# Performance work log

Hardware: AMD Instinct MI355X
Metric: run time of the kernel (lower is better)

## Reference

```python
import jax, jax.numpy as jnp
import numpy as np

B, L, DIM = 2, 1024, 1024
H, DH = 16, 64          # n_heads, dim_per_head
GS = 1                  # group_size
T = 3 * GS              # triplet heads (last T heads, head_choice==0)
HN = H - T              # normal heads
DG = DH * GS            # triplet 'pseudo-head' dim
SCALE = 1.0 / np.sqrt(DH)


def setup_inputs() -> dict:
    key = jax.random.key(0)
    ks = jax.random.split(key, 12)
    s = 0.02
    return {
        'query': jax.random.normal(ks[0], (B, L, DIM), jnp.float32),
        'key':   jax.random.normal(ks[1], (B, L, DIM), jnp.float32),
        'value': jax.random.normal(ks[2], (B, L, DIM), jnp.float32),
        'mask':  jnp.ones((B, L), dtype=jnp.int32),
        'Wq': jax.random.normal(ks[3], (DIM, DIM), jnp.float32) * s,
        'bq': jnp.zeros((DIM,), jnp.float32),
        'Wk': jax.random.normal(ks[4], (DIM, DIM), jnp.float32) * s,
        'bk': jnp.zeros((DIM,), jnp.float32),
        'Wv': jax.random.normal(ks[5], (DIM, DIM), jnp.float32) * s,
        'bv': jnp.zeros((DIM,), jnp.float32),
        'Wo': jax.random.normal(ks[6], (DIM, DIM), jnp.float32) * s,
        'bo': jnp.zeros((DIM,), jnp.float32),
    }


def _split_heads(x, W, b):
    # x: [B,L,DIM] -> [B,H,L,DH]
    return (x @ W.T + b).reshape(B, L, H, DH).transpose(0, 2, 1, 3)


def _triplet_reshape(x):
    # [B,T,L,DH] -> [B,L,T,DH] -> [B,L,DG,3] -> [B,DG,L,3]
    return x.transpose(0, 2, 1, 3).reshape(B, L, DG, 3).transpose(0, 2, 1, 3)


def reference(query, key, value, mask, Wq, bq, Wk, bk, Wv, bv, Wo, bo):
    q = _split_heads(query, Wq, bq)
    k = _split_heads(key, Wk, bk)
    v = _split_heads(value, Wv, bv)

    # head split: last T heads go to the triplet branch (head_choice == 0)
    qn, qt = q[:, :HN], q[:, HN:]
    kn, kt = k[:, :HN], k[:, HN:]
    vn, vt = v[:, :HN], v[:, HN:]

    # ---- triplet branch (layer in Tlayers) ----
    qtr = _triplet_reshape(qt)   # [B,DG,L,3]
    ktr = _triplet_reshape(kt)
    vtr = _triplet_reshape(vt)

    # key2_flag==1: key_triplet2 = clone; permute_type=[2] => roll index by 1 along L
    idx = jnp.roll(jnp.arange(L), 1)
    kt2 = ktr[:, :, idx, :]
    K_cross = jnp.cross(ktr, kt2, axis=-1)                 # [B,DG,L,3]

    attn_t = jnp.einsum('bdlt,bdmt->bdlm', qtr, K_cross)   # [B,DG,L,L]
    # permute_back==0, random_flag==0: inverse permutation along last dim
    inv = jnp.argsort(idx)
    attn_t = attn_t[..., inv]
    # absolute_flag==1
    attn_t = jnp.abs(attn_t)

    # ---- normal attention ----
    scores = jnp.einsum('bhld,bhmd->bhlm', qn * SCALE, kn)  # [B,HN,L,L]
    pad = (mask == 0)[:, None, None, :]
    scores = jnp.where(pad, -jnp.inf, scores)
    w = jax.nn.softmax(scores, axis=-1)                     # dropout p=0

    wt = jax.nn.softmax(attn_t * SCALE, axis=-1)            # [B,DG,L,L]

    ctx = jnp.einsum('bhlm,bhmd->bhld', w, vn)              # [B,HN,L,DH]
    ctx = ctx.transpose(0, 2, 1, 3).reshape(B, L, HN * DH)

    ctx_t = jnp.einsum('bdlm,bdmt->bdlt', wt, vtr)          # [B,DG,L,3]
    ctx_t = ctx_t.transpose(0, 2, 1, 3).reshape(B, L, DG * 3)

    context = jnp.concatenate([ctx, ctx_t], axis=-1)        # [B,L,DIM]
    return context @ Wo.T + bo
```

## Files before the change

kernel.cpp:

```cpp
#include <hip/hip_runtime.h>

#define L_SEQ 1024
typedef unsigned short ush;
typedef __attribute__((ext_vector_type(8))) short short8;
typedef __attribute__((ext_vector_type(4))) float f32x4;

#define MFMA __builtin_amdgcn_mfma_f32_16x16x32_bf16

#define Q_PRESCALE 0.18033688011112042f

__device__ __forceinline__ ush f2bf(float x) {
  union { float f; unsigned u; } c; c.f = x;
  unsigned r = c.u + 0x7FFF + ((c.u >> 16) & 1);
  return (ush)(r >> 16);
}
__device__ __forceinline__ float bf2f(ush h) {
  union { unsigned u; float f; } c; c.u = ((unsigned)h) << 16;
  return c.f;
}
__device__ __forceinline__ void gload16(const void* g, void* l) {
  __builtin_amdgcn_global_load_lds(
      (const __attribute__((address_space(1))) unsigned*)g,
      (__attribute__((address_space(3))) unsigned*)l, 16, 0, 0);
}

struct SplitA {
  const float* s0; const float* s1; const float* s2; const float* s3;
  const float* s4; const float* s5; const float* s6;
  ush* d0; ush* d1; ush* d2; ush* d3; ush* d4; ush* d5; ush* d6;
};
__global__ __launch_bounds__(256) void split_all(SplitA a) {
  const int ti = blockIdx.y;
  const float* s; ush* d; int n;
  switch (ti) {
    case 0: s = a.s0; d = a.d0; n = 1 << 21; break;
    case 1: s = a.s1; d = a.d1; n = 1 << 21; break;
    case 2: s = a.s2; d = a.d2; n = 1 << 21; break;
    case 3: s = a.s3; d = a.d3; n = 1 << 20; break;
    case 4: s = a.s4; d = a.d4; n = 1 << 20; break;
    case 5: s = a.s5; d = a.d5; n = 1 << 20; break;
    default: s = a.s6; d = a.d6; n = 1 << 20; break;
  }
  int i = (blockIdx.x * 256 + threadIdx.x) * 8;
  if (i >= n) return;
  float4 x0 = *(const float4*)(s + i);
  float4 x1 = *(const float4*)(s + i + 4);
  float xs[8] = {x0.x, x0.y, x0.z, x0.w, x1.x, x1.y, x1.z, x1.w};
  ush h[8], l[8];
  #pragma unroll
  for (int j = 0; j < 8; j++) {
    h[j] = f2bf(xs[j]);
    l[j] = f2bf(xs[j] - bf2f(h[j]));
  }
  ushort4 h0 = {h[0], h[1], h[2], h[3]}, h1 = {h[4], h[5], h[6], h[7]};
  ushort4 l0 = {l[0], l[1], l[2], l[3]}, l1 = {l[4], l[5], l[6], l[7]};
  *(ushort4*)(d + i) = h0;     *(ushort4*)(d + i + 4) = h1;
  *(ushort4*)(d + n + i) = l0; *(ushort4*)(d + n + i + 4) = l1;
}

template <int DBUF>
__global__ __launch_bounds__(256) void gemm_sp(
    const ush* __restrict__ Abase, long AzStride, long Aplane,
    const ush* __restrict__ Bbase, long BzStride,
    const float* __restrict__ b0, const float* __restrict__ b1,
    const float* __restrict__ b2,
    float* __restrict__ Yf, ush* __restrict__ Pbase) {
  __shared__ __align__(16) ush lds[DBUF ? 49152 : 24576];
  const int t = threadIdx.x;
  const int z = blockIdx.z;
  const ush* A = Abase + (size_t)z * AzStride;
  const ush* B = Bbase + (size_t)z * BzStride;
  const float* bias = (z == 0) ? b0 : (z == 1) ? b1 : b2;
  const long Bplane = 1024 * 1024;
  const int r0 = blockIdx.x * 128;
  const int n0 = blockIdx.y * 64;
  const int wid = t >> 6, lane = t & 63;
  const int wr = wid >> 1, wc = wid & 1;
  const int sr = t >> 3, ss = t & 7;
  const int sd = ss ^ (sr & 7);
  const int fr = lane & 15, fk = lane >> 4;

  f32x4 acc[4][2];
  #pragma unroll
  for (int mf = 0; mf < 4; mf++)
    #pragma unroll
    for (int nf = 0; nf < 2; nf++)
      acc[mf][nf] = (f32x4){0.f, 0.f, 0.f, 0.f};

  const ush* Ag = A + (size_t)(r0 + sr) * 1024 + sd * 8;
  const ush* Bg = B + (size_t)(n0 + sr) * 1024 + sd * 8;

  auto stage = [&](ush* Lb, int k0) {
    #pragma unroll
    for (int p = 0; p < 2; p++)
      #pragma unroll
      for (int c = 0; c < 4; c++)
        gload16(Ag + (size_t)p * Aplane + (size_t)c * 32 * 1024 + k0,
                Lb + p * 8192 + (c * 256 + t) * 8);
    #pragma unroll
    for (int p = 0; p < 2; p++)
      #pragma unroll
      for (int c = 0; c < 2; c++)
        gload16(Bg + (size_t)p * Bplane + (size_t)c * 32 * 1024 + k0,
                Lb + 16384 + p * 4096 + (c * 256 + t) * 8);
  };
  auto compute = [&](const ush* Lb) {
    #pragma unroll
    for (int g = 0; g < 2; g++) {
      short8 ah[4], al[4], bh[2], bl[2];
      const int sl = ((g * 4 + fk) ^ (fr & 7)) * 8;
      #pragma unroll
      for (int mf = 0; mf < 4; mf++) {
        int row = wr * 64 + mf * 16 + fr;
        ah[mf] = *(const short8*)(Lb + row * 64 + sl);
        al[mf] = *(const short8*)(Lb + 8192 + row * 64 + sl);
      }
      #pragma unroll
      for (int nf = 0; nf < 2; nf++) {
        int row = wc * 32 + nf * 16 + fr;
        bh[nf] = *(const short8*)(Lb + 16384 + row * 64 + sl);
        bl[nf] = *(const short8*)(Lb + 20480 + row * 64 + sl);
      }
      #pragma unroll
      for (int mf = 0; mf < 4; mf++)
        #pragma unroll
        for (int nf = 0; nf < 2; nf++) {
          acc[mf][nf] = MFMA(ah[mf], bh[nf], acc[mf][nf], 0, 0, 0);
          acc[mf][nf] = MFMA(ah[mf], bl[nf], acc[mf][nf], 0, 0, 0);
          acc[mf][nf] = MFMA(al[mf], bh[nf], acc[mf][nf], 0, 0, 0);
        }
    }
  };

  if constexpr (DBUF) {
    stage(lds, 0);
    __syncthreads();
    for (int k0 = 0; k0 < 1024; k0 += 64) {
      const int cur = (k0 >> 6) & 1;
      if (k0 + 64 < 1024) stage(lds + (cur ^ 1) * 24576, k0 + 64);
      compute(lds + cur * 24576);
      __syncthreads();
    }
  } else {
    for (int k0 = 0; k0 < 1024; k0 += 64) {
      __syncthreads();
      stage(lds, k0);
      __syncthreads();
      compute(lds);
    }
  }

  const float oscale = (z == 0) ? Q_PRESCALE : 1.0f;
  ush* Ph = Pbase ? (Pbase + (size_t)z * 4194304) : (ush*)0;
  ush* Pl = Ph ? Ph + 2097152 : (ush*)0;
  #pragma unroll
  for (int nf = 0; nf < 2; nf++) {
    const int col = n0 + wc * 32 + nf * 16 + fr;
    const float bb = bias[col];
    #pragma unroll
    for (int mf = 0; mf < 4; mf++) {
      const int rowb = r0 + wr * 64 + mf * 16 + fk * 4;
      if (Yf) {
        #pragma unroll
        for (int r = 0; r < 4; r++)
          Yf[(size_t)(rowb + r) * 1024 + col] = acc[mf][nf][r] + bb;
      } else if (z != 2) {
        #pragma unroll
        for (int r = 0; r < 4; r++) {
          float v = (acc[mf][nf][r] + bb) * oscale;
          ush hv = f2bf(v);
          Ph[(size_t)(rowb + r) * 1024 + col] = hv;
          Pl[(size_t)(rowb + r) * 1024 + col] = f2bf(v - bf2f(hv));
        }
      } else {
        ushort4 hv;
        #pragma unroll
        for (int r = 0; r < 4; r++)
          ((ush*)&hv)[r] = f2bf(acc[mf][nf][r] + bb);
        *(ushort4*)&Ph[(size_t)col * 2048 + rowb] = hv;
      }
    }
  }
}

__global__ __launch_bounds__(256) void trip_kc(
    const ush* __restrict__ kh, const ush* __restrict__ kl,
    ush* __restrict__ kc4g) {
  const int t = threadIdx.x;
  const int m = blockIdx.x * 256 + t;
  const int d = blockIdx.y, b = blockIdx.z;
  const int col = 832 + 3 * d;
  size_t r0 = (size_t)(b * 1024 + m) * 1024 + col;
  size_t r1 = (size_t)(b * 1024 + ((m + 1) & 1023)) * 1024 + col;
  float c0 = bf2f(kh[r0]) + bf2f(kl[r0]);
  float c1 = bf2f(kh[r0 + 1]) + bf2f(kl[r0 + 1]);
  float c2 = bf2f(kh[r0 + 2]) + bf2f(kl[r0 + 2]);
  float a0 = bf2f(kh[r1]) + bf2f(kl[r1]);
  float a1 = bf2f(kh[r1 + 1]) + bf2f(kl[r1 + 1]);
  float a2 = bf2f(kh[r1 + 2]) + bf2f(kl[r1 + 2]);
  ushort4 o;
  o.x = f2bf(a1 * c2 - a2 * c1);
  o.y = f2bf(a2 * c0 - a0 * c2);
  o.z = f2bf(a0 * c1 - a1 * c0);
  o.w = 0;
  *(ushort4*)(kc4g + ((size_t)(b * 64 + d) * 1024 + m) * 4) = o;
}

struct NormLds {
  ush Kh[2][4096];
  ush Kl[2][4096];
  ush Vt[2][4096];
  unsigned Pb[4][16][20];
};
struct TripLds {
  ush KC[4096];
  ush VT[4 * 1040];
  ush PB[4][16][36];
};
union FusedLds { NormLds n; TripLds t; };

__global__ __launch_bounds__(256) void attn_fused(
    const ush* __restrict__ qh, const ush* __restrict__ ql,
    const ush* __restrict__ kh, const ush* __restrict__ kl,
    const ush* __restrict__ vth, const ush* __restrict__ kc4g,
    ush* __restrict__ ctxh, ush* __restrict__ ctxl) {
  __shared__ __align__(16) FusedLds L;
  const int t = threadIdx.x;
  const int bid = blockIdx.x;
  const int lane = t & 63, w = t >> 6;
  const int c = lane & 15, g = lane >> 4;

  if (bid < 416) {
    const int l0 = (bid & 15) * 64;
    const int rem = bid >> 4;
    const int h = rem % 13, b = rem / 13;
    const int hoff = h * 64;
    const int srow = t >> 3, sg = t & 7;

    short8 ah[2], al[2];
    {
      size_t qbase = (size_t)(b * 1024 + l0 + w * 16 + c) * 1024 + hoff + g * 8;
      ah[0] = *(const short8*)(qh + qbase);
      ah[1] = *(const short8*)(qh + qbase + 32);
      al[0] = *(const short8*)(ql + qbase);
      al[1] = *(const short8*)(ql + qbase + 32);
    }
    auto stageKV = [&](int buf, int m0) {
      #pragma unroll
      for (int cc = 0; cc < 2; cc++) {
        int row = cc * 32 + srow;
        int slot = sg ^ (row & 7);
        size_t srck = (size_t)(b * 1024 + m0 + row) * 1024 + hoff + slot * 8;
        gload16(kh + srck, &L.n.Kh[buf][row * 64 + sg * 8]);
        gload16(kl + srck, &L.n.Kl[buf][row * 64 + sg * 8]);
        size_t srcv = (size_t)(hoff + row) * 2048 + b * 1024 + m0 + slot * 8;
        gload16(vth + srcv, &L.n.Vt[buf][row * 64 + sg * 8]);
      }
    };
    stageKV(0, 0);
    __syncthreads();

    const short8 ones = {0x3F80, 0x3F80, 0x3F80, 0x3F80,
                         0x3F80, 0x3F80, 0x3F80, 0x3F80};
    f32x4 acc[4];
    f32x4 accD = {0.f, 0.f, 0.f, 0.f};
    #pragma unroll
    for (int df = 0; df < 4; df++) acc[df] = (f32x4){0.f, 0.f, 0.f, 0.f};

    for (int step = 0; step < 16; step++) {
      const int cur = step & 1;
      if (step < 15) stageKV(cur ^ 1, (step + 1) * 64);
      const ush* KhC = &L.n.Kh[cur][0];
      const ush* KlC = &L.n.Kl[cur][0];
      const ush* VtC = &L.n.Vt[cur][0];
      f32x4 s[4];
      #pragma unroll
      for (int nf = 0; nf < 4; nf++) {
        s[nf] = (f32x4){0.f, 0.f, 0.f, 0.f};
        #pragma unroll
        for (int kk = 0; kk < 2; kk++) {
          int kr = nf * 16 + c;
          int slot = (kk * 4 + g) ^ (kr & 7);
          short8 bh = *(const short8*)(KhC + kr * 64 + slot * 8);
          short8 bl = *(const short8*)(KlC + kr * 64 + slot * 8);
          s[nf] = MFMA(bh, ah[kk], s[nf], 0, 0, 0);
          s[nf] = MFMA(bh, al[kk], s[nf], 0, 0, 0);
          s[nf] = MFMA(bl, ah[kk], s[nf], 0, 0, 0);
        }
      }
      float pr[4][4];
      #pragma unroll
      for (int nf = 0; nf < 4; nf++)
        #pragma unroll
        for (int r = 0; r < 4; r++) pr[nf][r] = exp2f(s[nf][r]);
      #pragma unroll
      for (int kk = 0; kk < 2; kk++) {
        #pragma unroll
        for (int nn = 0; nn < 2; nn++) {
          const int nf = kk * 2 + nn;
          unsigned u0, u1;
          asm("v_cvt_pk_bf16_f32 %0, %1, %2" : "=v"(u0) : "v"(pr[nf][0]), "v"(pr[nf][1]));
          asm("v_cvt_pk_bf16_f32 %0, %1, %2" : "=v"(u1) : "v"(pr[nf][2]), "v"(pr[nf][3]));
          *(uint2*)&L.n.Pb[w][c][nn * 8 + g * 2] = (uint2){u0, u1};
        }
        short8 pa = *(const short8*)&L.n.Pb[w][c][g * 4];
        accD = MFMA(pa, ones, accD, 0, 0, 0);
        #pragma unroll
        for (int df = 0; df < 4; df++) {
          int dr = df * 16 + c;
          int slot = (kk * 4 + g) ^ (dr & 7);
          short8 bv = *(const short8*)(VtC + dr * 64 + slot * 8);
          acc[df] = MFMA(pa, bv, acc[df], 0, 0, 0);
        }
      }
      __syncthreads();
    }
    float inv[4];
    #pragma unroll
    for (int r = 0; r < 4; r++) inv[r] = 1.0f / accD[r];
    #pragma unroll
    for (int df = 0; df < 4; df++)
      #pragma unroll
      for (int r = 0; r < 4; r++) {
        float o = acc[df][r] * inv[r];
        size_t off = (size_t)(b * 1024 + l0 + w * 16 + g * 4 + r) * 1024 + hoff + df * 16 + c;
        ush hv = f2bf(o);
        ctxh[off] = hv;
        ctxl[off] = f2bf(o - bf2f(hv));
      }
  } else {
    const int t2 = bid - 416;
    const int l0 = (t2 & 15) * 64;
    const int d = (t2 >> 4) & 63, b = t2 >> 10;
    const int col = 832 + 3 * d;

    const ush* kcsrc = kc4g + (size_t)(b * 64 + d) * 4096;
    gload16(kcsrc + t * 8, L.t.KC + t * 8);
    gload16(kcsrc + 2048 + t * 8, L.t.KC + 2048 + t * 8);

    {
      int row = t >> 6, chunk = t & 63;
      ush* dst = L.t.VT + row * 1040 + chunk * 16;
      if (row < 3) {
        const ush* src = vth + (size_t)(col + row) * 2048 + b * 1024 + chunk * 16;
        uint4 v0 = *(const uint4*)(src);
        uint4 v1 = *(const uint4*)(src + 8);
        *(uint4*)(dst) = v0;
        *(uint4*)(dst + 8) = v1;
      } else {
        uint4 onesv = {0x3F803F80u, 0x3F803F80u, 0x3F803F80u, 0x3F803F80u};
        *(uint4*)(dst) = onesv;
        *(uint4*)(dst + 8) = onesv;
      }
    }

    short8 qB = {0, 0, 0, 0, 0, 0, 0, 0};
    {
      size_t qr = (size_t)(b * 1024 + l0 + w * 16 + c) * 1024 + col;
      float q0 = bf2f(qh[qr]) + bf2f(ql[qr]);
      float q1 = bf2f(qh[qr + 1]) + bf2f(ql[qr + 1]);
      float q2 = bf2f(qh[qr + 2]) + bf2f(ql[qr + 2]);
      if (g == 0) {
        qB[0] = (short)f2bf(q0);
        qB[1] = (short)f2bf(q1);
        qB[2] = (short)f2bf(q2);
      }
    }
    __syncthreads();

    f32x4 acc = {0.f, 0.f, 0.f, 0.f};
    ush* pb = &L.t.PB[w][0][0];
    #pragma unroll 2
    for (int m0 = 0; m0 < 1024; m0 += 32) {
      short8 a0 = {0, 0, 0, 0, 0, 0, 0, 0}, a1 = {0, 0, 0, 0, 0, 0, 0, 0};
      *(uint2*)&a0 = *(const uint2*)(L.t.KC + (m0 + c) * 4);
      *(uint2*)&a1 = *(const uint2*)(L.t.KC + (m0 + 16 + c) * 4);
      f32x4 z = {0.f, 0.f, 0.f, 0.f};
      f32x4 s0 = MFMA(a0, qB, z, 0, 0, 0);
      f32x4 s1 = MFMA(a1, qB, z, 0, 0, 0);
      float p0 = exp2f(fabsf(s0[0])), p1 = exp2f(fabsf(s0[1]));
      float p2 = exp2f(fabsf(s0[2])), p3 = exp2f(fabsf(s0[3]));
      float p4 = exp2f(fabsf(s1[0])), p5 = exp2f(fabsf(s1[1]));
      float p6 = exp2f(fabsf(s1[2])), p7 = exp2f(fabsf(s1[3]));
      unsigned k01, k23, k45, k67;
      asm("v_cvt_pk_bf16_f32 %0, %1, %2" : "=v"(k01) : "v"(p0), "v"(p1));
      asm("v_cvt_pk_bf16_f32 %0, %1, %2" : "=v"(k23) : "v"(p2), "v"(p3));
      asm("v_cvt_pk_bf16_f32 %0, %1, %2" : "=v"(k45) : "v"(p4), "v"(p5));
      asm("v_cvt_pk_bf16_f32 %0, %1, %2" : "=v"(k67) : "v"(p6), "v"(p7));
      *(uint2*)(pb + c * 36 + 4 * g) = (uint2){k01, k23};
      *(uint2*)(pb + c * 36 + 16 + 4 * g) = (uint2){k45, k67};
      short8 pf;
      *(uint2*)&pf = *(const uint2*)(pb + c * 36 + 8 * g);
      *((uint2*)&pf + 1) = *(const uint2*)(pb + c * 36 + 8 * g + 4);
      short8 vf = *(const short8*)(L.t.VT + (c & 3) * 1040 + m0 + 8 * g);
      acc = MFMA(vf, pf, acc, 0, 0, 0);
    }
    if (g == 0) {
      const float inv = 1.0f / acc[3];
      size_t off = (size_t)(b * 1024 + l0 + w * 16 + c) * 1024 + col;
      #pragma unroll
      for (int comp = 0; comp < 3; comp++) {
        float o = acc[comp] * inv;
        ush hv = f2bf(o);
        ctxh[off + comp] = hv;
        ctxl[off + comp] = f2bf(o - bf2f(hv));
      }
    }
  }
}

extern "C" void kernel_launch(void* const* d_in, const int* in_sizes, int n_in,
                              void* d_out, int out_size, void* d_ws, size_t ws_size,
                              hipStream_t stream) {
  const float* query = (const float*)d_in[0];
  const float* key   = (const float*)d_in[1];
  const float* value = (const float*)d_in[2];
  const float* Wq = (const float*)d_in[4];
  const float* bq = (const float*)d_in[5];
  const float* Wk = (const float*)d_in[6];
  const float* bk = (const float*)d_in[7];
  const float* Wv = (const float*)d_in[8];
  const float* bv = (const float*)d_in[9];
  const float* Wo = (const float*)d_in[10];
  const float* bo = (const float*)d_in[11];
  float* out = (float*)d_out;

  char* W = (char*)d_ws;
  const size_t MB = 1 << 20;
  ush* qs  = (ush*)(W + 0 * MB);
  ush* ks  = (ush*)(W + 8 * MB);
  ush* vs  = (ush*)(W + 16 * MB);
  ush* Wqs = (ush*)(W + 24 * MB);
  ush* Wks = (ush*)(W + 28 * MB);
  ush* Wvs = (ush*)(W + 32 * MB);
  ush* Wos = (ush*)(W + 36 * MB);
  ush* planes = (ush*)(W + 40 * MB);
  ush* qh  = planes;
  ush* ql  = planes + 2097152;
  ush* khp = planes + 4194304;
  ush* klp = planes + 6291456;
  ush* vth = planes + 8388608;
  ush* ctxh = qs;
  ush* ctxl = qs + 2097152;
  ush* kc4g = ks;

  SplitA sa = {query, key, value, Wq, Wk, Wv, Wo,
               qs, ks, vs, Wqs, Wks, Wvs, Wos};
  split_all<<<dim3(1024, 7), 256, 0, stream>>>(sa);

  gemm_sp<0><<<dim3(16, 16, 3), 256, 0, stream>>>(
      qs, (long)(4 * 1024 * 1024), (long)(2 * 1024 * 1024),
      Wqs, (long)(2 * 1024 * 1024),
      bq, bk, bv,
      (float*)0, planes);

  trip_kc<<<dim3(4, 64, 2), 256, 0, stream>>>(khp, klp, kc4g);

  attn_fused<<<dim3(416 + 2048), 256, 0, stream>>>(
      qh, ql, khp, klp, vth, kc4g, ctxh, ctxl);

  gemm_sp<1><<<dim3(16, 16, 1), 256, 0, stream>>>(
      ctxh, 0L, (long)(2 * 1024 * 1024),
      Wos, 0L,
      bo, bo, bo,
      out, (ush*)0);
}
```

Baseline: 158.7 us.

## Drop K/V double buffering in normal-attention path; double-buffer triplet P tiles

The normal-attention branch goes from double-buffered K/V LDS staging to single buffering. Each step now syncs, loads the tile, syncs again, then computes. This roughly halves the LDS footprint of that branch and may allow more resident blocks per CU. The cost is that global-to-LDS loads no longer overlap the MFMA work, and each step now has two barriers. The triplet branch separately alternates between two P scratch buffers across iterations, likely to avoid write-after-read hazards without an extra barrier.

Result: faster. 147.1 us (median of 2 runs) (-7.3%).

```diff
diff --git a/kernel.cpp b/kernel.cpp
--- a/kernel.cpp
+++ b/kernel.cpp
@@ -207,15 +207,15 @@
 }
 
 struct NormLds {
-  ush Kh[2][4096];
-  ush Kl[2][4096];
-  ush Vt[2][4096];
+  ush Kh[4096];
+  ush Kl[4096];
+  ush Vt[4096];
   unsigned Pb[4][16][20];
 };
 struct TripLds {
   ush KC[4096];
   ush VT[4 * 1040];
-  ush PB[4][16][36];
+  ush PB[4][2][16][36];
 };
 union FusedLds { NormLds n; TripLds t; };
 
@@ -245,20 +245,18 @@
       al[0] = *(const short8*)(ql + qbase);
       al[1] = *(const short8*)(ql + qbase + 32);
     }
-    auto stageKV = [&](int buf, int m0) {
+    auto stageKV = [&](int m0) {
       #pragma unroll
       for (int cc = 0; cc < 2; cc++) {
         int row = cc * 32 + srow;
         int slot = sg ^ (row & 7);
         size_t srck = (size_t)(b * 1024 + m0 + row) * 1024 + hoff + slot * 8;
-        gload16(kh + srck, &L.n.Kh[buf][row * 64 + sg * 8]);
-        gload16(kl + srck, &L.n.Kl[buf][row * 64 + sg * 8]);
+        gload16(kh + srck, &L.n.Kh[row * 64 + sg * 8]);
+        gload16(kl + srck, &L.n.Kl[row * 64 + sg * 8]);
         size_t srcv = (size_t)(hoff + row) * 2048 + b * 1024 + m0 + slot * 8;
-        gload16(vth + srcv, &L.n.Vt[buf][row * 64 + sg * 8]);
+        gload16(vth + srcv, &L.n.Vt[row * 64 + sg * 8]);
       }
     };
-    stageKV(0, 0);
-    __syncthreads();
 
     const short8 ones = {0x3F80, 0x3F80, 0x3F80, 0x3F80,
                          0x3F80, 0x3F80, 0x3F80, 0x3F80};
@@ -268,11 +266,9 @@
     for (int df = 0; df < 4; df++) acc[df] = (f32x4){0.f, 0.f, 0.f, 0.f};
 
     for (int step = 0; step < 16; step++) {
-      const int cur = step & 1;
-      if (step < 15) stageKV(cur ^ 1, (step + 1) * 64);
-      const ush* KhC = &L.n.Kh[cur][0];
-      const ush* KlC = &L.n.Kl[cur][0];
-      const ush* VtC = &L.n.Vt[cur][0];
+      if (step > 0) __syncthreads();
+      stageKV(step * 64);
+      __syncthreads();
       f32x4 s[4];
       #pragma unroll
       for (int nf = 0; nf < 4; nf++) {
@@ -281,8 +277,8 @@
         for (int kk = 0; kk < 2; kk++) {
           int kr = nf * 16 + c;
           int slot = (kk * 4 + g) ^ (kr & 7);
-          short8 bh = *(const short8*)(KhC + kr * 64 + slot * 8);
-          short8 bl = *(const short8*)(KlC + kr * 64 + slot * 8);
+          short8 bh = *(const short8*)(&L.n.Kh[kr * 64 + slot * 8]);
+          short8 bl = *(const short8*)(&L.n.Kl[kr * 64 + slot * 8]);
           s[nf] = MFMA(bh, ah[kk], s[nf], 0, 0, 0);
           s[nf] = MFMA(bh, al[kk], s[nf], 0, 0, 0);
           s[nf] = MFMA(bl, ah[kk], s[nf], 0, 0, 0);
@@ -309,11 +305,10 @@
         for (int df = 0; df < 4; df++) {
           int dr = df * 16 + c;
           int slot = (kk * 4 + g) ^ (dr & 7);
-          short8 bv = *(const short8*)(VtC + dr * 64 + slot * 8);
+          short8 bv = *(const short8*)(&L.n.Vt[dr * 64 + slot * 8]);
           acc[df] = MFMA(pa, bv, acc[df], 0, 0, 0);
         }
       }
-      __syncthreads();
     }
     float inv[4];
     #pragma unroll
@@ -369,9 +364,9 @@
     __syncthreads();
 
     f32x4 acc = {0.f, 0.f, 0.f, 0.f};
-    ush* pb = &L.t.PB[w][0][0];
     #pragma unroll 2
     for (int m0 = 0; m0 < 1024; m0 += 32) {
+      ush* pb = &L.t.PB[w][(m0 >> 5) & 1][0][0];
       short8 a0 = {0, 0, 0, 0, 0, 0, 0, 0}, a1 = {0, 0, 0, 0, 0, 0, 0, 0};
       *(uint2*)&a0 = *(const uint2*)(L.t.KC + (m0 + c) * 4);
       *(uint2*)&a1 = *(const uint2*)(L.t.KC + (m0 + 16 + c) * 4);
```
